# Kernel tuning notes

Hardware: AMD Instinct MI355X
Metric: run time of the kernel (lower is better)

## Reference

```python
import jax, jax.numpy as jnp
import numpy as np

HIDDEN = 2048
N_EXPERTS = 8
TOP_K = 2
MOE_INTER = 1408
NORM_TOPK = False  # config.norm_topk_prob


def setup_inputs() -> dict:
    key = jax.random.key(0)
    k0, k1, k2, k3, k4 = jax.random.split(key, 5)
    hidden_states = jax.random.normal(k0, (2, 2048, HIDDEN), dtype=jnp.float32)
    # router gate: nn.Linear(hidden, num_experts, bias=False) -> store as [H, E]
    gate_w = jax.random.normal(k1, (HIDDEN, N_EXPERTS), dtype=jnp.float32) * 0.02
    # per-expert MLP weights, stacked over experts (Linear is x @ W.T, stored pre-transposed)
    w_gate = jax.random.normal(k2, (N_EXPERTS, HIDDEN, MOE_INTER), dtype=jnp.float32) * 0.02
    w_up = jax.random.normal(k3, (N_EXPERTS, HIDDEN, MOE_INTER), dtype=jnp.float32) * 0.02
    w_down = jax.random.normal(k4, (N_EXPERTS, MOE_INTER, HIDDEN), dtype=jnp.float32) * 0.02
    return {"hidden_states": hidden_states, "gate_w": gate_w,
            "w_gate": w_gate, "w_up": w_up, "w_down": w_down}


def reference(hidden_states, gate_w, w_gate, w_up, w_down):
    B, S, H = hidden_states.shape
    x = hidden_states.reshape(-1, H)                      # [T, H]
    T = x.shape[0]
    router_logits = x @ gate_w                            # [T, E]
    probs = jax.nn.softmax(router_logits.astype(jnp.float32), axis=-1)
    routing_weights, selected = jax.lax.top_k(probs, TOP_K)  # [T, K], [T, K]
    if NORM_TOPK:
        routing_weights = routing_weights / routing_weights.sum(-1, keepdims=True)
    routing_weights = routing_weights.astype(x.dtype)
    # dense combine weights [T, E]: scatter top-k weights to expert slots
    combine = jnp.zeros((T, N_EXPERTS), dtype=x.dtype)
    combine = combine.at[jnp.arange(T)[:, None], selected].add(routing_weights)
    # run all experts densely (reference form of gather-MLP-scatter)
    g = jnp.einsum('th,ehf->tef', x, w_gate)              # [T, E, F]
    u = jnp.einsum('th,ehf->tef', x, w_up)
    h = jax.nn.silu(g) * u
    y = jnp.einsum('tef,efh->teh', h, w_down)             # [T, E, H]
    out = jnp.einsum('te,teh->th', combine, y)            # [T, H]
    return out
```

## Files before the change

kernel.cpp:

```cpp
#include <hip/hip_runtime.h>
#include <hip/hip_bf16.h>

#define HID  2048
#define NEXP 8
#define FINT 1408
#define TM   128
#define BK   32
#define GU_NPAN 88
#define DN_NPAN 64
#define NG_GU (NEXP * 11 * 64)
#define NG_DN (NEXP * 8 * 44)

typedef __bf16 bf16_t;
typedef __bf16 bf16x8 __attribute__((ext_vector_type(8)));
typedef float  f32x4  __attribute__((ext_vector_type(4)));

#define AS1 __attribute__((address_space(1)))
#define AS3 __attribute__((address_space(3)))

__device__ __forceinline__ void gll16(const void* g, void* l) {
    __builtin_amdgcn_global_load_lds((const AS1 void*)g, (AS3 void*)l, 16, 0, 0);
}

#define VMCNT6() asm volatile("s_waitcnt vmcnt(6)" ::: "memory")
#define VMCNT0() asm volatile("s_waitcnt vmcnt(0)" ::: "memory")
#define SB0() __builtin_amdgcn_sched_barrier(0)

__device__ __forceinline__ unsigned pack2(float a, float b) {
    bf16_t x = (bf16_t)a, y = (bf16_t)b;
    unsigned short ux, uy;
    __builtin_memcpy(&ux, &x, 2);
    __builtin_memcpy(&uy, &y, 2);
    return (unsigned)ux | ((unsigned)uy << 16);
}

__global__ __launch_bounds__(256) void prep_kernel(
    const float* __restrict__ x, const float* __restrict__ gw,
    int* __restrict__ cnt, int* __restrict__ topk_id, float* __restrict__ topk_w,
    bf16_t* __restrict__ xb, int T,
    const float* __restrict__ wg, const float* __restrict__ wu, const float* __restrict__ wd,
    bf16_t* __restrict__ wB, bf16_t* __restrict__ wD)
{
    const int RB = T / 4;
    __shared__ unsigned lds[256][20];

    if ((int)blockIdx.x < RB) {
        int tid = threadIdx.x;
        int lane = tid & 63, w = tid >> 6;
        int t = blockIdx.x * 4 + w;
        if (t >= T) return;
        float acc[NEXP];
#pragma unroll
        for (int e = 0; e < NEXP; ++e) acc[e] = 0.f;
        const float* xr = x + (size_t)t * HID;
        bf16_t* xo = xb + (size_t)t * HID;
        for (int i0 = lane * 4; i0 < HID; i0 += 256) {
            float4 xv = *(const float4*)(xr + i0);
            bf16_t b4[4] = {(bf16_t)xv.x, (bf16_t)xv.y, (bf16_t)xv.z, (bf16_t)xv.w};
            *(uint2*)(xo + i0) = *(uint2*)b4;
            float xs[4] = {xv.x, xv.y, xv.z, xv.w};
#pragma unroll
            for (int u = 0; u < 4; ++u) {
                const float4* g4 = (const float4*)(gw + (size_t)(i0 + u) * NEXP);
                float4 a = g4[0], b = g4[1];
                acc[0] += xs[u] * a.x; acc[1] += xs[u] * a.y; acc[2] += xs[u] * a.z; acc[3] += xs[u] * a.w;
                acc[4] += xs[u] * b.x; acc[5] += xs[u] * b.y; acc[6] += xs[u] * b.z; acc[7] += xs[u] * b.w;
            }
        }
#pragma unroll
        for (int d = 1; d < 64; d <<= 1) {
#pragma unroll
            for (int e = 0; e < NEXP; ++e) acc[e] += __shfl_xor(acc[e], d, 64);
        }
        float mx = acc[0];
#pragma unroll
        for (int e = 1; e < NEXP; ++e) mx = fmaxf(mx, acc[e]);
        float p[NEXP]; float s = 0.f;
#pragma unroll
        for (int e = 0; e < NEXP; ++e) { p[e] = expf(acc[e] - mx); s += p[e]; }
        float inv = 1.f / s;
        int i1 = 0;
#pragma unroll
        for (int e = 1; e < NEXP; ++e) if (acc[e] > acc[i1]) i1 = e;
        int i2 = (i1 == 0) ? 1 : 0;
#pragma unroll
        for (int e = 0; e < NEXP; ++e) if (e != i1 && acc[e] > acc[i2]) i2 = e;
        if (lane == 0) {
            topk_id[t * 2 + 0] = i1; topk_id[t * 2 + 1] = i2;
            topk_w[t * 2 + 0] = p[i1] * inv; topk_w[t * 2 + 1] = p[i2] * inv;
            atomicAdd(&cnt[i1], 1); atomicAdd(&cnt[i2], 1);
        }
        return;
    }

    int b = blockIdx.x - RB;
    int t = threadIdx.x;
    bf16_t* dst16;

    if (b < NG_GU) {
        int e = b / 704, rem = b - e * 704;
        int fp = rem / 64, kt = rem - fp * 64;
        int tp = t & 127;
        const float* W = (t < 128) ? wg : wu;
        int rbase = (t < 128) ? 0 : 128;
        const float* src = W + ((size_t)e * HID + kt * 32) * FINT + fp * 128;
#pragma unroll
        for (int r = 0; r < 4; ++r) {
            int kp = ((tp >> 4) & 7) | ((r & 1) << 3);
            int f  = ((tp & 15) | ((r >> 1) << 4)) * 4;
            const float* s0 = src + (size_t)(2 * kp) * FINT + f;
            float4 a  = *(const float4*)s0;
            float4 bb = *(const float4*)(s0 + FINT);
            lds[rbase + f + 0][kp] = pack2(a.x, bb.x);
            lds[rbase + f + 1][kp] = pack2(a.y, bb.y);
            lds[rbase + f + 2][kp] = pack2(a.z, bb.z);
            lds[rbase + f + 3][kp] = pack2(a.w, bb.w);
        }
        dst16 = wB + (size_t)b * 8192 + t * 32;
    } else {
        int b2 = b - NG_GU;
        int e = b2 / 352, rem = b2 - e * 352;
        int hp = rem / 44, kt = rem - hp * 44;
        const float* src = wd + ((size_t)e * FINT + kt * 32) * HID + hp * 256;
        int kp = t >> 4;
#pragma unroll
        for (int r = 0; r < 4; ++r) {
            int h = ((t & 15) + 16 * r) * 4;
            const float* s0 = src + (size_t)(2 * kp) * HID + h;
            float4 a  = *(const float4*)s0;
            float4 bb = *(const float4*)(s0 + HID);
            lds[h + 0][kp] = pack2(a.x, bb.x);
            lds[h + 1][kp] = pack2(a.y, bb.y);
            lds[h + 2][kp] = pack2(a.z, bb.z);
            lds[h + 3][kp] = pack2(a.w, bb.w);
        }
        dst16 = wD + (size_t)b2 * 8192 + t * 32;
    }
    __syncthreads();

    int swz = ((t & 15) >> 1) & 3;
    uint4* dst = (uint4*)dst16;
#pragma unroll
    for (int c = 0; c < 4; ++c)
        dst[c] = *(const uint4*)&lds[t][(c ^ swz) * 4];
}

__global__ void offsets_kernel(const int* __restrict__ cnt, int* __restrict__ offs,
                               int* __restrict__ gbase, int* __restrict__ gcount,
                               int* __restrict__ dbase, int* __restrict__ dcount,
                               int* __restrict__ gu, int* __restrict__ dn)
{
    __shared__ int gc[8], dc[8];
    int tid = threadIdx.x;
    if (tid == 0) {
        int s = 0;
        for (int e = 0; e < NEXP; ++e) { offs[e] = s; s += cnt[e]; }
        offs[NEXP] = s;
    }
    if (tid < 8) {
        int c = 0;
        for (int p = tid; p < GU_NPAN; p += 8) { int e = p / 11; c += (cnt[e] + TM - 1) / TM; }
        gc[tid] = c;
    } else if (tid < 16) {
        int x = tid - 8, c = 0;
        for (int p = x; p < DN_NPAN; p += 8) { int e = p >> 3; c += (cnt[e] + TM - 1) / TM; }
        dc[x] = c;
    }
    __syncthreads();
    if (tid < 8) {
        int base = 0;
        for (int i = 0; i < tid; ++i) base += gc[i];
        gbase[tid] = base; gcount[tid] = gc[tid];
        int k = base;
        for (int p = tid; p < GU_NPAN; p += 8) {
            int e = p / 11, fp = p - e * 11;
            int nt = (cnt[e] + TM - 1) / TM;
            for (int t = 0; t < nt; ++t) gu[k++] = (e << 10) | (fp << 6) | t;
        }
    } else if (tid < 16) {
        int x = tid - 8;
        int base = 0;
        for (int i = 0; i < x; ++i) base += dc[i];
        dbase[x] = base; dcount[x] = dc[x];
        int k = base;
        for (int p = x; p < DN_NPAN; p += 8) {
            int e = p >> 3, hp = p & 7;
            int nt = (cnt[e] + TM - 1) / TM;
            for (int t = 0; t < nt; ++t) dn[k++] = (e << 10) | (hp << 6) | t;
        }
    }
}

__global__ void scatter_kernel(
    const int* __restrict__ topk_id, const int* __restrict__ offs, int* __restrict__ fill,
    int* __restrict__ tok, int* __restrict__ slot_of, int T)
{
    int t = blockIdx.x * blockDim.x + threadIdx.x;
    if (t >= T) return;
#pragma unroll
    for (int k = 0; k < 2; ++k) {
        int e = topk_id[t * 2 + k];
        int pos = atomicAdd(&fill[e], 1);
        int slot = offs[e] + pos;
        tok[slot] = t;
        slot_of[t * 2 + k] = slot;
    }
}

__global__ __launch_bounds__(256, 2) void gateup3_kernel(
    const bf16_t* __restrict__ xb, const bf16_t* __restrict__ wB,
    const int* __restrict__ offs, const int* __restrict__ tok,
    const int* __restrict__ gbase, const int* __restrict__ gcount, const int* __restrict__ gu,
    bf16_t* __restrict__ h_buf)
{
    __shared__ bf16_t smem[36864];
    const int tid = threadIdx.x;
    const int lane = tid & 63, w = tid >> 6;
    const int lr = lane & 15, lg = lane >> 4;
    const int rl = lane >> 2;
    const int sw8 = ((lane & 3) ^ ((lane >> 3) & 3)) * 8;
    const int ksw = (lg ^ ((lr >> 1) & 3)) * 8;

    const int xcd = blockIdx.x & 7, slot = blockIdx.x >> 3;
    const int icnt = gcount[xcd], ib = gbase[xcd];

    for (int ii = slot; ii < icnt; ii += 88) {
        const int it = gu[ib + ii];
        const int e = it >> 10, fp = (it >> 6) & 15, tr = it & 63;
        const int seg0 = offs[e];
        const int rbase = tr * TM;
        const int nvalid = min(offs[e + 1] - seg0 - rbase, TM);
        const int row0 = seg0 + rbase;
        const int f0 = fp * 128;

        const bf16_t* aP[2];
#pragma unroll
        for (int i = 0; i < 2; ++i) {
            int r = w * 32 + i * 16 + rl;
            int tk = tok[row0 + min(r, nvalid - 1)];
            aP[i] = xb + (size_t)tk * HID + sw8;
        }
        const bf16_t* bT = wB + (size_t)(e * 11 + fp) * 64 * 8192 + lane * 8;

        f32x4 acc[8][4];
#pragma unroll
        for (int mi = 0; mi < 8; ++mi)
#pragma unroll
            for (int ni = 0; ni < 4; ++ni) acc[mi][ni] = (f32x4){0.f, 0.f, 0.f, 0.f};

        auto STAGE = [&](int b, int kt) {
            int k0 = kt * BK;
            bf16_t* A = smem + b * 4096;
            bf16_t* B = smem + 12288 + b * 8192;
            gll16(aP[0] + k0, A + (w * 2 + 0) * 512);
            gll16(aP[1] + k0, A + (w * 2 + 1) * 512);
            const bf16_t* bk = bT + (size_t)kt * 8192;
            gll16(bk + (w * 4 + 0) * 512, B + (w * 4 + 0) * 512);
            gll16(bk + (w * 4 + 1) * 512, B + (w * 4 + 1) * 512);
            gll16(bk + (w * 4 + 2) * 512, B + (w * 4 + 2) * 512);
            gll16(bk + (w * 4 + 3) * 512, B + (w * 4 + 3) * 512);
        };
        auto COMPUTE = [&](int b) {
            const bf16_t* A = smem + b * 4096;
            const bf16_t* B = smem + 12288 + b * 8192;
            bf16x8 bfr[4];
#pragma unroll
            for (int ni = 0; ni < 4; ++ni)
                bfr[ni] = *(const bf16x8*)&B[(w * 64 + ni * 16 + lr) * BK + ksw];
#pragma unroll
            for (int mi = 0; mi < 8; ++mi) {
                bf16x8 a = *(const bf16x8*)&A[(mi * 16 + lr) * BK + ksw];
#pragma unroll
                for (int ni = 0; ni < 4; ++ni)
                    acc[mi][ni] = __builtin_amdgcn_mfma_f32_16x16x32_bf16(a, bfr[ni], acc[mi][ni], 0, 0, 0);
            }
        };

        const int NK = HID / BK;
        STAGE(0, 0); STAGE(1, 1);
        int c0 = 0, c1 = 1, c2 = 2;
        for (int kt = 0; kt < NK - 1; ++kt) {
            SB0(); VMCNT6(); __builtin_amdgcn_s_barrier(); SB0();
            if (kt + 2 < NK) STAGE(c2, kt + 2);
            SB0();
            COMPUTE(c0);
            int t = c0; c0 = c1; c1 = c2; c2 = t;
        }
        SB0(); VMCNT0(); __builtin_amdgcn_s_barrier(); SB0();
        COMPUTE(c0);
        __syncthreads();

        if (w >= 2) {
#pragma unroll
            for (int mi = 0; mi < 8; ++mi)
#pragma unroll
                for (int ni = 0; ni < 4; ++ni)
#pragma unroll
                    for (int rr = 0; rr < 4; ++rr) {
                        int row = mi * 16 + lg * 4 + rr;
                        int col = (w - 2) * 64 + ni * 16 + lr;
                        smem[row * 128 + col] = (bf16_t)acc[mi][ni][rr];
                    }
        }
        __syncthreads();
        if (w < 2) {
#pragma unroll
            for (int mi = 0; mi < 8; ++mi)
#pragma unroll
                for (int ni = 0; ni < 4; ++ni)
#pragma unroll
                    for (int rr = 0; rr < 4; ++rr) {
                        int row = mi * 16 + lg * 4 + rr;
                        int col = w * 64 + ni * 16 + lr;
                        float g = acc[mi][ni][rr];
                        float u = (float)smem[row * 128 + col];
                        float h = (g / (1.f + __expf(-g))) * u;
                        if (row < nvalid)
                            h_buf[(size_t)(row0 + row) * FINT + f0 + col] = (bf16_t)h;
                    }
        }
        __syncthreads();
    }
}

__global__ __launch_bounds__(256, 2) void down3_kernel(
    const bf16_t* __restrict__ h_buf, const bf16_t* __restrict__ wD,
    const int* __restrict__ offs,
    const int* __restrict__ dbase, const int* __restrict__ dcount, const int* __restrict__ dn,
    bf16_t* __restrict__ y_buf)
{
    __shared__ bf16_t smem[36864];
    const int tid = threadIdx.x;
    const int lane = tid & 63, w = tid >> 6;
    const int lr = lane & 15, lg = lane >> 4;
    const int rl = lane >> 2;
    const int sw8 = ((lane & 3) ^ ((lane >> 3) & 3)) * 8;
    const int ksw = (lg ^ ((lr >> 1) & 3)) * 8;

    const int xcd = blockIdx.x & 7, slot = blockIdx.x >> 3;
    const int icnt = dcount[xcd], ib = dbase[xcd];

    for (int ii = slot; ii < icnt; ii += 64) {
        const int it = dn[ib + ii];
        const int e = it >> 10, hp = (it >> 6) & 15, tr = it & 63;
        const int seg0 = offs[e];
        const int rbase = tr * TM;
        const int nvalid = min(offs[e + 1] - seg0 - rbase, TM);
        const int row0 = seg0 + rbase;
        const int h0 = hp * 256;

        const bf16_t* aP[2];
#pragma unroll
        for (int i = 0; i < 2; ++i) {
            int r = w * 32 + i * 16 + rl;
            aP[i] = h_buf + (size_t)(row0 + min(r, nvalid - 1)) * FINT + sw8;
        }
        const bf16_t* bT = wD + (size_t)(e * 8 + hp) * 44 * 8192 + lane * 8;

        f32x4 acc[8][4];
#pragma unroll
        for (int mi = 0; mi < 8; ++mi)
#pragma unroll
            for (int ni = 0; ni < 4; ++ni) acc[mi][ni] = (f32x4){0.f, 0.f, 0.f, 0.f};

        auto STAGE = [&](int b, int kt) {
            int k0 = kt * BK;
            bf16_t* A = smem + b * 4096;
            bf16_t* B = smem + 12288 + b * 8192;
            gll16(aP[0] + k0, A + (w * 2 + 0) * 512);
            gll16(aP[1] + k0, A + (w * 2 + 1) * 512);
            const bf16_t* bk = bT + (size_t)kt * 8192;
            gll16(bk + (w * 4 + 0) * 512, B + (w * 4 + 0) * 512);
            gll16(bk + (w * 4 + 1) * 512, B + (w * 4 + 1) * 512);
            gll16(bk + (w * 4 + 2) * 512, B + (w * 4 + 2) * 512);
            gll16(bk + (w * 4 + 3) * 512, B + (w * 4 + 3) * 512);
        };
        auto COMPUTE = [&](int b) {
            const bf16_t* A = smem + b * 4096;
            const bf16_t* B = smem + 12288 + b * 8192;
            bf16x8 bfr[4];
#pragma unroll
            for (int ni = 0; ni < 4; ++ni)
                bfr[ni] = *(const bf16x8*)&B[(w * 64 + ni * 16 + lr) * BK + ksw];
#pragma unroll
            for (int mi = 0; mi < 8; ++mi) {
                bf16x8 a = *(const bf16x8*)&A[(mi * 16 + lr) * BK + ksw];
#pragma unroll
                for (int ni = 0; ni < 4; ++ni)
                    acc[mi][ni] = __builtin_amdgcn_mfma_f32_16x16x32_bf16(a, bfr[ni], acc[mi][ni], 0, 0, 0);
            }
        };

        const int NK = FINT / BK;
        STAGE(0, 0); STAGE(1, 1);
        int c0 = 0, c1 = 1, c2 = 2;
        for (int kt = 0; kt < NK - 1; ++kt) {
            SB0(); VMCNT6(); __builtin_amdgcn_s_barrier(); SB0();
            if (kt + 2 < NK) STAGE(c2, kt + 2);
            SB0();
            COMPUTE(c0);
            int t = c0; c0 = c1; c1 = c2; c2 = t;
        }
        SB0(); VMCNT0(); __builtin_amdgcn_s_barrier(); SB0();
        COMPUTE(c0);

#pragma unroll
        for (int mi = 0; mi < 8; ++mi)
#pragma unroll
            for (int ni = 0; ni < 4; ++ni)
#pragma unroll
                for (int rr = 0; rr < 4; ++rr) {
                    int row = mi * 16 + lg * 4 + rr;
                    int col = w * 64 + ni * 16 + lr;
                    if (row < nvalid)
                        y_buf[(size_t)(row0 + row) * HID + h0 + col] = (bf16_t)acc[mi][ni][rr];
                }
        __syncthreads();
    }
}

__global__ __launch_bounds__(256) void combine_kernel(
    const bf16_t* __restrict__ y, const int* __restrict__ slot_of,
    const float* __restrict__ topk_w, float* __restrict__ out, int T)
{
    int t = blockIdx.x;
    int tid = threadIdx.x;
    int s0 = slot_of[t * 2], s1 = slot_of[t * 2 + 1];
    float w0 = topk_w[t * 2], w1 = topk_w[t * 2 + 1];
    const bf16x8* y0 = (const bf16x8*)(y + (size_t)s0 * HID);
    const bf16x8* y1 = (const bf16x8*)(y + (size_t)s1 * HID);
    bf16x8 v0 = y0[tid], v1 = y1[tid];
    float* op = out + (size_t)t * HID + tid * 8;
#pragma unroll
    for (int j = 0; j < 8; ++j)
        op[j] = w0 * (float)v0[j] + w1 * (float)v1[j];
}

extern "C" void kernel_launch(void* const* d_in, const int* in_sizes, int n_in,
                              void* d_out, int out_size, void* d_ws, size_t ws_size,
                              hipStream_t stream)
{
    const float* x  = (const float*)d_in[0];
    const float* gw = (const float*)d_in[1];
    const float* wg = (const float*)d_in[2];
    const float* wu = (const float*)d_in[3];
    const float* wd = (const float*)d_in[4];
    float* out = (float*)d_out;
    int T = in_sizes[0] / HID;
    int S2 = 2 * T;

    char* base = (char*)d_ws;
    int* cnt     = (int*)base;
    int* fill    = cnt + 8;
    int* offs    = cnt + 16;
    int* gbase   = cnt + 32;
    int* gcount  = cnt + 40;
    int* dbase   = cnt + 48;
    int* dcount  = cnt + 56;
    int* gu      = cnt + 64;
    int* dnl     = cnt + 1088;
    int* topk_id = cnt + 1856;
    float* topk_w = (float*)(topk_id + S2);
    int* tok     = (int*)(topk_w + S2);
    int* slot_of = tok + S2 + 256;
    size_t small_end = (size_t)((char*)(slot_of + S2) - base);
    size_t cur = (small_end + 255) & ~(size_t)255;
    auto take = [&](size_t bytes) -> size_t {
        size_t o = cur; cur += bytes; cur = (cur + 255) & ~(size_t)255; return o;
    };
    size_t o_xb = take((size_t)T * HID * 2);
    size_t o_wB = take((size_t)NG_GU * 8192 * 2);
    size_t o_wD = take((size_t)NG_DN * 8192 * 2);
    size_t o_h  = take((size_t)(S2 + 256) * FINT * 2);
    size_t o_y  = take((size_t)(S2 + 256) * HID * 2);
    (void)ws_size;

    bf16_t* xb    = (bf16_t*)(base + o_xb);
    bf16_t* wB    = (bf16_t*)(base + o_wB);
    bf16_t* wD    = (bf16_t*)(base + o_wD);
    bf16_t* h_buf = (bf16_t*)(base + o_h);
    bf16_t* y_buf = (bf16_t*)(base + o_y);

    hipMemsetAsync(base, 0, 64, stream);

    int RB = T / 4;
    int gridPrep = RB + NG_GU + NG_DN;
    prep_kernel<<<gridPrep, 256, 0, stream>>>(x, gw, cnt, topk_id, topk_w, xb, T,
                                              wg, wu, wd, wB, wD);
    offsets_kernel<<<1, 64, 0, stream>>>(cnt, offs, gbase, gcount, dbase, dcount, gu, dnl);
    scatter_kernel<<<(T + 255) / 256, 256, 0, stream>>>(topk_id, offs, fill, tok, slot_of, T);

    gateup3_kernel<<<704, 256, 0, stream>>>(xb, wB, offs, tok, gbase, gcount, gu, h_buf);
    down3_kernel<<<512, 256, 0, stream>>>(h_buf, wD, offs, dbase, dcount, dnl, y_buf);
    combine_kernel<<<T, 256, 0, stream>>>(y_buf, slot_of, topk_w, out, T);
}
```

Baseline: 438.5 us.

## Move down-projection weight conversion into gate/up kernel as extra blocks

The fp32-to-bf16 repacking of the down-projection weights moves out of the prep kernel and into extra blocks appended to the gate/up GEMM grid. Those blocks can then run alongside the GEMM tiles rather than in front of them on the critical path. The cost is a larger GEMM grid, and the conversion blocks compete with GEMM blocks for bandwidth and CU slots, which may perturb the XCD-based scheduling of GEMM tiles.

Measured after the change: 417.8 us (median of 2 runs). 4.7% less time.

```diff
diff --git a/kernel.cpp b/kernel.cpp
--- a/kernel.cpp
+++ b/kernel.cpp
@@ -10,6 +10,7 @@
 #define DN_NPAN 64
 #define NG_GU (NEXP * 11 * 64)
 #define NG_DN (NEXP * 8 * 44)
+#define GU_GRID 704
 
 typedef __bf16 bf16_t;
 typedef __bf16 bf16x8 __attribute__((ext_vector_type(8)));
@@ -38,8 +39,8 @@
     const float* __restrict__ x, const float* __restrict__ gw,
     int* __restrict__ cnt, int* __restrict__ topk_id, float* __restrict__ topk_w,
     bf16_t* __restrict__ xb, int T,
-    const float* __restrict__ wg, const float* __restrict__ wu, const float* __restrict__ wd,
-    bf16_t* __restrict__ wB, bf16_t* __restrict__ wD)
+    const float* __restrict__ wg, const float* __restrict__ wu,
+    bf16_t* __restrict__ wB)
 {
     const int RB = T / 4;
     __shared__ unsigned lds[256][20];
@@ -95,51 +96,29 @@
 
     int b = blockIdx.x - RB;
     int t = threadIdx.x;
-    bf16_t* dst16;
-
-    if (b < NG_GU) {
-        int e = b / 704, rem = b - e * 704;
-        int fp = rem / 64, kt = rem - fp * 64;
-        int tp = t & 127;
-        const float* W = (t < 128) ? wg : wu;
-        int rbase = (t < 128) ? 0 : 128;
-        const float* src = W + ((size_t)e * HID + kt * 32) * FINT + fp * 128;
-#pragma unroll
-        for (int r = 0; r < 4; ++r) {
-            int kp = ((tp >> 4) & 7) | ((r & 1) << 3);
-            int f  = ((tp & 15) | ((r >> 1) << 4)) * 4;
-            const float* s0 = src + (size_t)(2 * kp) * FINT + f;
-            float4 a  = *(const float4*)s0;
-            float4 bb = *(const float4*)(s0 + FINT);
-            lds[rbase + f + 0][kp] = pack2(a.x, bb.x);
-            lds[rbase + f + 1][kp] = pack2(a.y, bb.y);
-            lds[rbase + f + 2][kp] = pack2(a.z, bb.z);
-            lds[rbase + f + 3][kp] = pack2(a.w, bb.w);
-        }
-        dst16 = wB + (size_t)b * 8192 + t * 32;
-    } else {
-        int b2 = b - NG_GU;
-        int e = b2 / 352, rem = b2 - e * 352;
-        int hp = rem / 44, kt = rem - hp * 44;
-        const float* src = wd + ((size_t)e * FINT + kt * 32) * HID + hp * 256;
-        int kp = t >> 4;
-#pragma unroll
-        for (int r = 0; r < 4; ++r) {
-            int h = ((t & 15) + 16 * r) * 4;
-            const float* s0 = src + (size_t)(2 * kp) * HID + h;
-            float4 a  = *(const float4*)s0;
-            float4 bb = *(const float4*)(s0 + HID);
-            lds[h + 0][kp] = pack2(a.x, bb.x);
-            lds[h + 1][kp] = pack2(a.y, bb.y);
-            lds[h + 2][kp] = pack2(a.z, bb.z);
-            lds[h + 3][kp] = pack2(a.w, bb.w);
-        }
-        dst16 = wD + (size_t)b2 * 8192 + t * 32;
+
+    int e = b / 704, rem = b - e * 704;
+    int fp = rem / 64, kt = rem - fp * 64;
+    int tp = t & 127;
+    const float* W = (t < 128) ? wg : wu;
+    int rbase = (t < 128) ? 0 : 128;
+    const float* src = W + ((size_t)e * HID + kt * 32) * FINT + fp * 128;
+#pragma unroll
+    for (int r = 0; r < 4; ++r) {
+        int kp = ((tp >> 4) & 7) | ((r & 1) << 3);
+        int f  = ((tp & 15) | ((r >> 1) << 4)) * 4;
+        const float* s0 = src + (size_t)(2 * kp) * FINT + f;
+        float4 a  = *(const float4*)s0;
+        float4 bb = *(const float4*)(s0 + FINT);
+        lds[rbase + f + 0][kp] = pack2(a.x, bb.x);
+        lds[rbase + f + 1][kp] = pack2(a.y, bb.y);
+        lds[rbase + f + 2][kp] = pack2(a.z, bb.z);
+        lds[rbase + f + 3][kp] = pack2(a.w, bb.w);
     }
     __syncthreads();
 
     int swz = ((t & 15) >> 1) & 3;
-    uint4* dst = (uint4*)dst16;
+    uint4* dst = (uint4*)(wB + (size_t)b * 8192 + t * 32);
 #pragma unroll
     for (int c = 0; c < 4; ++c)
         dst[c] = *(const uint4*)&lds[t][(c ^ swz) * 4];
@@ -211,10 +190,40 @@
     const bf16_t* __restrict__ xb, const bf16_t* __restrict__ wB,
     const int* __restrict__ offs, const int* __restrict__ tok,
     const int* __restrict__ gbase, const int* __restrict__ gcount, const int* __restrict__ gu,
-    bf16_t* __restrict__ h_buf)
+    bf16_t* __restrict__ h_buf,
+    const float* __restrict__ wd, bf16_t* __restrict__ wD)
 {
     __shared__ bf16_t smem[36864];
     const int tid = threadIdx.x;
+
+    if ((int)blockIdx.x >= GU_GRID) {
+        unsigned (*lds)[20] = (unsigned(*)[20])smem;
+        int b2 = (int)blockIdx.x - GU_GRID;
+        int t = tid;
+        int e = b2 / 352, rem = b2 - e * 352;
+        int hp = rem / 44, kt = rem - hp * 44;
+        const float* src = wd + ((size_t)e * FINT + kt * 32) * HID + hp * 256;
+        int kp = t >> 4;
+#pragma unroll
+        for (int r = 0; r < 4; ++r) {
+            int h = ((t & 15) + 16 * r) * 4;
+            const float* s0 = src + (size_t)(2 * kp) * HID + h;
+            float4 a  = *(const float4*)s0;
+            float4 bb = *(const float4*)(s0 + HID);
+            lds[h + 0][kp] = pack2(a.x, bb.x);
+            lds[h + 1][kp] = pack2(a.y, bb.y);
+            lds[h + 2][kp] = pack2(a.z, bb.z);
+            lds[h + 3][kp] = pack2(a.w, bb.w);
+        }
+        __syncthreads();
+        int swz = ((t & 15) >> 1) & 3;
+        uint4* dst = (uint4*)(wD + (size_t)b2 * 8192 + t * 32);
+#pragma unroll
+        for (int c = 0; c < 4; ++c)
+            dst[c] = *(const uint4*)&lds[t][(c ^ swz) * 4];
+        return;
+    }
+
     const int lane = tid & 63, w = tid >> 6;
     const int lr = lane & 15, lg = lane >> 4;
     const int rl = lane >> 2;
@@ -484,13 +493,14 @@
     hipMemsetAsync(base, 0, 64, stream);
 
     int RB = T / 4;
-    int gridPrep = RB + NG_GU + NG_DN;
+    int gridPrep = RB + NG_GU;
     prep_kernel<<<gridPrep, 256, 0, stream>>>(x, gw, cnt, topk_id, topk_w, xb, T,
-                                              wg, wu, wd, wB, wD);
+                                              wg, wu, wB);
     offsets_kernel<<<1, 64, 0, stream>>>(cnt, offs, gbase, gcount, dbase, dcount, gu, dnl);
     scatter_kernel<<<(T + 255) / 256, 256, 0, stream>>>(topk_id, offs, fill, tok, slot_of, T);
 
-    gateup3_kernel<<<704, 256, 0, stream>>>(xb, wB, offs, tok, gbase, gcount, gu, h_buf);
+    gateup3_kernel<<<GU_GRID + NG_DN, 256, 0, stream>>>(xb, wB, offs, tok, gbase, gcount, gu,
+                                                        h_buf, wd, wD);
     down3_kernel<<<512, 256, 0, stream>>>(h_buf, wD, offs, dbase, dcount, dnl, y_buf);
     combine_kernel<<<T, 256, 0, stream>>>(y_buf, slot_of, topk_w, out, T);
 }
```
